# Kernel optimization log

Measured on AMD Instinct MI355X. Metric: run time of the kernel, lower is better.

The kernel has to match this reference:

```python
import jax, jax.numpy as jnp
import numpy as np

B, Hh, Ww, C = 16, 56, 56, 384
HEADS, WS, SHIFT = 12, 7, 3
N = WS * WS            # 49 tokens per window
NW = (Hh // WS) * (Ww // WS)  # 64 windows
HID = int(C * 4.0)
SCALE = (C // HEADS) ** -0.5
EPS = 1e-5


def _relative_position_index():
    coords = np.stack(np.meshgrid(np.arange(WS), np.arange(WS), indexing='ij')).reshape(2, -1)
    rel = (coords[:, :, None] - coords[:, None, :]).transpose(1, 2, 0)  # (N,N,2)
    rel[..., 0] += WS - 1
    rel[..., 1] += WS - 1
    rel[..., 0] *= 2 * WS - 1
    return jnp.asarray(rel.sum(-1))  # (N,N) int

RPI = _relative_position_index()


def _swin_mask():
    img = np.zeros((Hh, Ww), np.float32)
    slices = (slice(0, -WS), slice(-WS, -SHIFT), slice(-SHIFT, None))
    cnt = 0
    for hs in slices:
        for ws in slices:
            img[hs, ws] = cnt
            cnt += 1
    m = img.reshape(Hh // WS, WS, Ww // WS, WS).transpose(0, 2, 1, 3).reshape(-1, N)  # (nW,N)
    am = m[:, None, :] - m[:, :, None]
    return jnp.asarray(np.where(am != 0, -100.0, 0.0).astype(np.float32))  # (nW,N,N)


def setup_inputs() -> dict:
    key = jax.random.key(0)
    ks = jax.random.split(key, 12)
    p = lambda k, shp, s=0.02: (jax.random.normal(k, shp, jnp.float32) * s)
    return {
        'x': jax.random.normal(ks[0], (B, Hh * Ww, C), jnp.float32),
        'mask_matrix': _swin_mask(),
        'norm1_g': jnp.ones((C,), jnp.float32),
        'norm1_b': jnp.zeros((C,), jnp.float32),
        'qkv_w': p(ks[1], (3 * C, C)),
        'qkv_b': jnp.zeros((3 * C,), jnp.float32),
        'rpb_table': p(ks[2], ((2 * WS - 1) * (2 * WS - 1), HEADS)),
        'proj_w': p(ks[3], (C, C)),
        'proj_b': jnp.zeros((C,), jnp.float32),
        'norm2_g': jnp.ones((C,), jnp.float32),
        'norm2_b': jnp.zeros((C,), jnp.float32),
        'fc1_w': p(ks[4], (HID, C)),
        'fc1_b': jnp.zeros((HID,), jnp.float32),
        'fc2_w': p(ks[5], (C, HID)),
        'fc2_b': jnp.zeros((C,), jnp.float32),
    }


def _ln(x, g, b):
    m = jnp.mean(x, -1, keepdims=True)
    v = jnp.mean(jnp.square(x - m), -1, keepdims=True)
    return (x - m) * jax.lax.rsqrt(v + EPS) * g + b


def reference(x, mask_matrix, norm1_g, norm1_b, qkv_w, qkv_b, rpb_table,
              proj_w, proj_b, norm2_g, norm2_b, fc1_w, fc1_b, fc2_w, fc2_b):
    shortcut = x
    h = _ln(x, norm1_g, norm1_b).reshape(B, Hh, Ww, C)
    # cyclic shift (H,W divisible by window -> no pad)
    h = jnp.roll(h, (-SHIFT, -SHIFT), axis=(1, 2))
    # window partition -> (B*nW, N, C)
    win = h.reshape(B, Hh // WS, WS, Ww // WS, WS, C).transpose(0, 1, 3, 2, 4, 5).reshape(-1, N, C)
    B_ = win.shape[0]
    hd = C // HEADS
    qkv = (win @ qkv_w.T + qkv_b).reshape(B_, N, 3, HEADS, hd).transpose(2, 0, 3, 1, 4)
    q, k, v = qkv[0] * SCALE, qkv[1], qkv[2]  # (B_,H,N,hd)
    attn = jnp.einsum('bhnd,bhmd->bhnm', q, k)  # (B_,H,N,N)
    bias = rpb_table[RPI]  # (N,N,heads)
    attn = attn + bias.transpose(2, 0, 1)[None]
    attn = attn.reshape(B, NW, HEADS, N, N) + mask_matrix[None, :, None]
    attn = jax.nn.softmax(attn.reshape(B_, HEADS, N, N), axis=-1)
    out = jnp.einsum('bhnm,bhmd->bhnd', attn, v).transpose(0, 2, 1, 3).reshape(B_, N, C)
    out = out @ proj_w.T + proj_b
    # window reverse + reverse shift
    out = out.reshape(B, Hh // WS, Ww // WS, WS, WS, C).transpose(0, 1, 3, 2, 4, 5).reshape(B, Hh, Ww, C)
    out = jnp.roll(out, (SHIFT, SHIFT), axis=(1, 2)).reshape(B, Hh * Ww, C)
    x = shortcut + out
    h2 = _ln(x, norm2_g, norm2_b)
    h2 = jax.nn.gelu(h2 @ fc1_w.T + fc1_b, approximate=False)  # torch nn.GELU exact
    return x + (h2 @ fc2_w.T + fc2_b)
```

## Files before the change

kernel.cpp:

```cpp
#include <hip/hip_runtime.h>

typedef unsigned short u16;
typedef unsigned int u32;
typedef short s16x8 __attribute__((ext_vector_type(8)));
typedef unsigned short u16x4 __attribute__((ext_vector_type(4)));
typedef float f32x4 __attribute__((ext_vector_type(4)));

#define ATTN_SCALE 0.17677669529663687f

__device__ __forceinline__ u16 f2bf(float f) {
  union { float f; u32 i; } c; c.f = f;
  u32 r = c.i + 0x7fffu + ((c.i >> 16) & 1u);
  return (u16)(r >> 16);
}
__device__ __forceinline__ float bf2f(u16 u) {
  union { u32 i; float f; } c; c.i = ((u32)u) << 16; return c.f;
}
__device__ __forceinline__ f32x4 mfma16(s16x8 a, s16x8 b, f32x4 c) {
  return __builtin_amdgcn_mfma_f32_16x16x32_bf16(a, b, c, 0, 0, 0);
}

typedef __attribute__((address_space(1))) u32 gas_u32;
typedef __attribute__((address_space(3))) u32 las_u32;
#define GLL16(gp, lp) __builtin_amdgcn_global_load_lds((gas_u32*)(gp), (las_u32*)(lp), 16, 0, 0)

__device__ __forceinline__ int win_to_orig(int m) {
  int b = m / 3136, rem = m - b * 3136;
  int w = rem / 49, n = rem - w * 49;
  int wh = w >> 3, ww = w & 7;
  int i = n / 7, j = n - i * 7;
  int r = wh * 7 + i + 3; if (r >= 56) r -= 56;
  int c = ww * 7 + j + 3; if (c >= 56) c -= 56;
  return b * 3136 + r * 56 + c;
}

__global__ __launch_bounds__(256) void cvt_all_kernel(
    const float* __restrict__ qkvw, const float* __restrict__ projw,
    const float* __restrict__ fc1w, const float* __restrict__ fc2w,
    u16* __restrict__ wq, u16* __restrict__ wp,
    u16* __restrict__ w1, u16* __restrict__ w2) {
  int i = blockIdx.x * 256 + threadIdx.x;
  if (i < 442368) wq[i] = f2bf(qkvw[i]);
  else if (i < 589824) wp[i - 442368] = f2bf(projw[i - 442368]);
  else if (i < 1179648) w1[i - 589824] = f2bf(fc1w[i - 589824]);
  else if (i < 1769472) w2[i - 1179648] = f2bf(fc2w[i - 1179648]);
}

__global__ __launch_bounds__(256) void mk_tbl_kernel(
    const float* __restrict__ rpb, const float* __restrict__ maskp,
    u16* __restrict__ tbl) {
  int idx = blockIdx.x * 256 + threadIdx.x;
  int wh = idx >> 12;
  int rem = idx & 4095;
  int irow = rem >> 6;
  int lr = (rem >> 2) & 15, ni = rem & 3;
  int j = ni * 16 + lr;
  int wi = wh / 12, h = wh - wi * 12;
  float val = -1e30f;
  if (irow < 49 && j < 49) {
    int yi = irow / 7, xi = irow - yi * 7;
    int yj = j / 7, xj = j - yj * 7;
    int rpi = (yi - yj + 6) * 13 + (xi - xj + 6);
    val = rpb[rpi * 12 + h] + maskp[((size_t)wi * 49 + irow) * 49 + j];
  }
  tbl[idx] = f2bf(val);
}

template <bool PERM, bool BFIN>
__global__ __launch_bounds__(256) void ln_kernel(
    const void* __restrict__ xin, const float* __restrict__ g,
    const float* __restrict__ bb, u16* __restrict__ xo) {
  int t = blockIdx.x * 4 + (threadIdx.x >> 6);
  int l = threadIdx.x & 63;
  int src = PERM ? win_to_orig(t) : t;
  float v[6];
  if (BFIN) {
    const u16* row = (const u16*)xin + (size_t)src * 384;
#pragma unroll
    for (int k = 0; k < 6; k++) v[k] = bf2f(row[l + 64 * k]);
  } else {
    const float* row = (const float*)xin + (size_t)src * 384;
#pragma unroll
    for (int k = 0; k < 6; k++) v[k] = row[l + 64 * k];
  }
  float s = 0.f;
#pragma unroll
  for (int k = 0; k < 6; k++) s += v[k];
#pragma unroll
  for (int d = 1; d < 64; d <<= 1) s += __shfl_xor(s, d);
  float mean = s * (1.f / 384.f);
  float q = 0.f;
#pragma unroll
  for (int k = 0; k < 6; k++) { float dv = v[k] - mean; q += dv * dv; }
#pragma unroll
  for (int d = 1; d < 64; d <<= 1) q += __shfl_xor(q, d);
  float rstd = rsqrtf(q * (1.f / 384.f) + 1e-5f);
  u16* orow = xo + (size_t)t * 384;
#pragma unroll
  for (int k = 0; k < 6; k++) {
    int c = l + 64 * k;
    orow[c] = f2bf((v[k] - mean) * rstd * g[c] + bb[c]);
  }
}

template <int EPI>
__global__ __launch_bounds__(256) void gemm_kernel(
    const u16* __restrict__ A, const u16* __restrict__ W,
    const float* __restrict__ bias, u16* __restrict__ outb,
    float* __restrict__ outf, const float* __restrict__ auxf,
    const u16* __restrict__ auxb, int K, int N, int NT, int NB) {
  __shared__ __align__(16) short As[8192];
  __shared__ __align__(16) short Bs[8192];
  const int tid = threadIdx.x, wv = tid >> 6, l = tid & 63;
  const int lr = l & 15, lg = l >> 4;
  int bm, bn;
  {
    const int STS = NT << 3;
    const int body = (NB >> 3) * STS;
    int d = blockIdx.x;
    if (d < body) {
      int st = d / STS, rem = d - st * STS;
      bn = rem >> 3;
      bm = st * 8 + (rem & 7);
    } else {
      int t = d - body;
      int tq = t / NT;
      bm = (NB & ~7) + tq;
      bn = t - tq * NT;
    }
  }
  const size_t m0 = (size_t)bm * 128, n0 = (size_t)bn * 128;
  const int prow = wv * 16 + (l >> 2);
  const int ccl = (((l & 3) ^ ((l >> 3) & 3)) << 3);
  const u16* ga0 = A + (m0 + prow) * K + ccl;
  const u16* ga1 = A + (m0 + 64 + prow) * K + ccl;
  const u16* gb0 = W + (n0 + prow) * K + ccl;
  const u16* gb1 = W + (n0 + 64 + prow) * K + ccl;
  const int stoff = wv * 512;
  const int wr = wv >> 1, wc = wv & 1;
  const int sw = (lr >> 1) & 3;
  const int aoff = (wr * 64 + lr) * 32 + ((lg ^ sw) << 3);
  const int boff = (wc * 64 + lr) * 32 + ((lg ^ sw) << 3);

#define STAGE(bufo, koff)                            \
  do {                                               \
    GLL16(ga0 + (koff), As + (bufo) + stoff);        \
    GLL16(ga1 + (koff), As + (bufo) + 2048 + stoff); \
    GLL16(gb0 + (koff), Bs + (bufo) + stoff);        \
    GLL16(gb1 + (koff), Bs + (bufo) + 2048 + stoff); \
  } while (0)
#define FRAG_READS(cur)                                              \
  do {                                                               \
    const short* as = As + (cur);                                    \
    const short* bs = Bs + (cur);                                    \
    _Pragma("unroll") for (int mi = 0; mi < 4; mi++)                 \
        af[mi] = *(const s16x8*)&as[aoff + mi * (16 * 32)];          \
    _Pragma("unroll") for (int ni = 0; ni < 4; ni++)                 \
        bfr[ni] = *(const s16x8*)&bs[boff + ni * (16 * 32)];         \
  } while (0)
#define MFMA_TILE()                                        \
  do {                                                     \
    _Pragma("unroll") for (int mi = 0; mi < 4; mi++)       \
        _Pragma("unroll") for (int ni = 0; ni < 4; ni++)   \
            acc[mi][ni] = mfma16(af[mi], bfr[ni], acc[mi][ni]); \
  } while (0)

  f32x4 acc[4][4] = {};
  s16x8 af[4], bfr[4];
  STAGE(0, 0);
  STAGE(4096, 32);
  int cur = 0;
  int k0 = 0;
  for (; k0 < K - 32; k0 += 32) {
    asm volatile("s_waitcnt vmcnt(4)" ::: "memory");
    __builtin_amdgcn_sched_barrier(0);
    __builtin_amdgcn_s_barrier();
    FRAG_READS(cur);
    asm volatile("s_waitcnt lgkmcnt(0)" ::: "memory");
    __builtin_amdgcn_sched_barrier(0);
    __builtin_amdgcn_s_barrier();
    if (k0 + 64 < K) STAGE(cur, k0 + 64);
    MFMA_TILE();
    cur ^= 4096;
  }
  asm volatile("s_waitcnt vmcnt(0)" ::: "memory");
  __builtin_amdgcn_sched_barrier(0);
  __builtin_amdgcn_s_barrier();
  FRAG_READS(cur);
  asm volatile("s_waitcnt lgkmcnt(0)" ::: "memory");
  __builtin_amdgcn_sched_barrier(0);
  MFMA_TILE();
#undef STAGE
#undef FRAG_READS
#undef MFMA_TILE

  const int colb = (int)n0 + wc * 64;
#pragma unroll
  for (int mi = 0; mi < 4; mi++) {
#pragma unroll
    for (int r = 0; r < 4; r++) {
      const size_t m = m0 + wr * 64 + mi * 16 + lg * 4 + r;
      int dst = 0;
      if (EPI == 1) dst = win_to_orig((int)m);
#pragma unroll
      for (int ni = 0; ni < 4; ni++) {
        const int col = colb + ni * 16 + lr;
        float v = acc[mi][ni][r] + bias[col];
        if (EPI == 0) {
          outb[m * (size_t)N + col] = f2bf(v);
        } else if (EPI == 1) {
          outb[(size_t)dst * 384 + col] = f2bf(v + auxf[(size_t)dst * 384 + col]);
        } else if (EPI == 2) {
          float u = v * (0.7978845608028654f + 0.0356774081f * v * v);
          float gl = v / (1.f + __expf(-2.f * u));
          outb[m * (size_t)N + col] = f2bf(gl);
        } else {
          outf[m * (size_t)N + col] = v + bf2f(auxb[m * (size_t)N + col]);
        }
      }
    }
  }
}

__global__ __launch_bounds__(256) void attn_kernel(
    const u16* __restrict__ qkv, const u16* __restrict__ tbl,
    u16* __restrict__ out) {
  __shared__ __align__(16) short Pl[4][16 * 76];
  const int tid = threadIdx.x, wv = tid >> 6, l = tid & 63;
  const int lr = l & 15, lg = l >> 4;

  const int task = blockIdx.x * 4 + wv;
  const int win = task / 12, h = task - win * 12;
  const int wi = win & 63;
  const short* base = (const short*)qkv + (size_t)win * 49 * 1152 + h * 32;
  const u16* tb = tbl + (size_t)(wi * 12 + h) * 4096 + lr * 4;

  s16x8 qf[4], kf[4];
  const s16x8 zz = {0, 0, 0, 0, 0, 0, 0, 0};
#pragma unroll
  for (int mi = 0; mi < 4; mi++) {
    int n = mi * 16 + lr;
    if (n < 49) {
      qf[mi] = *(const s16x8*)(base + (size_t)n * 1152 + lg * 8);
      kf[mi] = *(const s16x8*)(base + (size_t)n * 1152 + 384 + lg * 8);
    } else { qf[mi] = zz; kf[mi] = zz; }
  }
  s16x8 vb[2][2];
#pragma unroll
  for (int kk = 0; kk < 2; kk++)
#pragma unroll
    for (int nd = 0; nd < 2; nd++)
#pragma unroll
      for (int e = 0; e < 8; e++)
        vb[kk][nd][e] = base[(size_t)(kk * 32 + lg * 8 + e) * 1152 + 768 + nd * 16 + lr];
  u16x4 t4[4][4];
#pragma unroll
  for (int r = 0; r < 4; r++)
    t4[0][r] = *(const u16x4*)&tb[(lg * 4 + r) * 64];

  f32x4 acc[4][4] = {};
  __builtin_amdgcn_s_setprio(1);
#pragma unroll
  for (int mi = 0; mi < 4; mi++)
#pragma unroll
    for (int ni = 0; ni < 4; ni++)
      acc[mi][ni] = mfma16(qf[mi], kf[ni], acc[mi][ni]);
  __builtin_amdgcn_s_setprio(0);

  short* pl = Pl[wv];
#pragma unroll
  for (int mi = 0; mi < 4; mi++) {
    if (mi < 3) {
#pragma unroll
      for (int r = 0; r < 4; r++)
        t4[mi + 1][r] = *(const u16x4*)&tb[((mi + 1) * 16 + lg * 4 + r) * 64];
    }
    float rs[4];
#pragma unroll
    for (int r = 0; r < 4; r++) {
      float sv[4];
#pragma unroll
      for (int ni = 0; ni < 4; ni++)
        sv[ni] = acc[mi][ni][r] * ATTN_SCALE + bf2f(t4[mi][r][ni]);
      float mx = fmaxf(fmaxf(sv[0], sv[1]), fmaxf(sv[2], sv[3]));
#pragma unroll
      for (int d = 1; d < 16; d <<= 1) mx = fmaxf(mx, __shfl_xor(mx, d));
      float sm = 0.f;
#pragma unroll
      for (int ni = 0; ni < 4; ni++) { sv[ni] = __expf(sv[ni] - mx); sm += sv[ni]; }
#pragma unroll
      for (int d = 1; d < 16; d <<= 1) sm += __shfl_xor(sm, d);
      rs[r] = 1.f / sm;
#pragma unroll
      for (int ni = 0; ni < 4; ni++)
        pl[(lg * 4 + r) * 76 + ni * 16 + lr] = (short)f2bf(sv[ni]);
    }
    f32x4 o[2] = {{}, {}};
    __builtin_amdgcn_s_setprio(1);
#pragma unroll
    for (int kk = 0; kk < 2; kk++) {
      s16x8 pa = *(const s16x8*)&pl[lr * 76 + kk * 32 + lg * 8];
#pragma unroll
      for (int nd = 0; nd < 2; nd++)
        o[nd] = mfma16(pa, vb[kk][nd], o[nd]);
    }
    __builtin_amdgcn_s_setprio(0);
#pragma unroll
    for (int r = 0; r < 4; r++) {
      const int irow = mi * 16 + lg * 4 + r;
      if (irow < 49) {
#pragma unroll
        for (int nd = 0; nd < 2; nd++)
          out[((size_t)win * 49 + irow) * 384 + h * 32 + nd * 16 + lr] =
              f2bf(o[nd][r] * rs[r]);
      }
    }
  }
}

extern "C" void kernel_launch(void* const* d_in, const int* in_sizes, int n_in,
                              void* d_out, int out_size, void* d_ws, size_t ws_size,
                              hipStream_t stream) {
  (void)in_sizes; (void)n_in; (void)out_size; (void)ws_size;
  const float* x     = (const float*)d_in[0];
  const float* maskp = (const float*)d_in[1];
  const float* n1g   = (const float*)d_in[2];
  const float* n1b   = (const float*)d_in[3];
  const float* qkvw  = (const float*)d_in[4];
  const float* qkvb  = (const float*)d_in[5];
  const float* rpb   = (const float*)d_in[6];
  const float* projw = (const float*)d_in[7];
  const float* projb = (const float*)d_in[8];
  const float* n2g   = (const float*)d_in[9];
  const float* n2b   = (const float*)d_in[10];
  const float* fc1w  = (const float*)d_in[11];
  const float* fc1b  = (const float*)d_in[12];
  const float* fc2w  = (const float*)d_in[13];
  const float* fc2b  = (const float*)d_in[14];
  float* outp = (float*)d_out;

  char* ws = (char*)d_ws;
  u16*  regA  = (u16*)ws;
  u16*  regB  = (u16*)(ws + 115605504ull);
  u16*  xresb = (u16*)(ws + 154140672ull);
  u16*  wq = (u16*)(ws + 192675840ull);
  u16*  wp = wq + 442368;
  u16*  w1 = wp + 147456;
  u16*  w2 = w1 + 589824;
  u16*  tbl = w2 + 589824;

  cvt_all_kernel<<<6912, 256, 0, stream>>>(qkvw, projw, fc1w, fc2w, wq, wp, w1, w2);
  mk_tbl_kernel<<<12288, 256, 0, stream>>>(rpb, maskp, tbl);
  ln_kernel<true, false><<<12544, 256, 0, stream>>>(x, n1g, n1b, regB);
  gemm_kernel<0><<<392 * 9, 256, 0, stream>>>(regB, wq, qkvb, regA, nullptr,
                                              nullptr, nullptr, 384, 1152, 9, 392);
  attn_kernel<<<3072, 256, 0, stream>>>(regA, tbl, regB);
  gemm_kernel<1><<<392 * 3, 256, 0, stream>>>(regB, wp, projb, xresb, nullptr,
                                              x, nullptr, 384, 384, 3, 392);
  ln_kernel<false, true><<<12544, 256, 0, stream>>>(xresb, n2g, n2b, regB);
  for (int c = 0; c < 2; c++) {
    const u16* aln = regB + (size_t)c * 25088 * 384;
    float* oc = outp + (size_t)c * 25088 * 384;
    const u16* rc = xresb + (size_t)c * 25088 * 384;
    gemm_kernel<2><<<196 * 12, 256, 0, stream>>>(aln, w1, fc1b, regA, nullptr,
                                                 nullptr, nullptr, 384, 1536, 12, 196);
    gemm_kernel<3><<<196 * 3, 256, 0, stream>>>(regA, w2, fc2b, nullptr, oc,
                                                nullptr, rc, 1536, 384, 3, 196);
  }
}
```

Baseline: 409.4 us.

## Add 256x128 GEMM tile variant and run MLP in one pass

Adds a 512-thread GEMM kernel with a 256x128 output tile (8x2 MFMA fragments per wave, setprio around the MFMA block). It is used for the QKV and FC1 GEMMs, while the proj and FC2 GEMMs keep the 128x128 kernel. The workspace is re-laid-out so the FC1 intermediate for all 50176 tokens fits, which removes the two-chunk MLP loop and halves the GEMM launch count there. The bias table and xresb now share a workspace offset, which is safe only because the table is dead after attention. The larger tile raises per-block reuse and register pressure but leaves fewer blocks per GEMM.

```diff
diff --git a/kernel.cpp b/kernel.cpp
--- a/kernel.cpp
+++ b/kernel.cpp
@@ -104,7 +104,25 @@
 }
 
 template <int EPI>
-__global__ __launch_bounds__(256) void gemm_kernel(
+__device__ __forceinline__ void gemm_epi(
+    float v, size_t m, int col, int N, int dst,
+    u16* __restrict__ outb, float* __restrict__ outf,
+    const float* __restrict__ auxf, const u16* __restrict__ auxb) {
+  if (EPI == 0) {
+    outb[m * (size_t)N + col] = f2bf(v);
+  } else if (EPI == 1) {
+    outb[(size_t)dst * 384 + col] = f2bf(v + auxf[(size_t)dst * 384 + col]);
+  } else if (EPI == 2) {
+    float u = v * (0.7978845608028654f + 0.0356774081f * v * v);
+    float gl = v / (1.f + __expf(-2.f * u));
+    outb[m * (size_t)N + col] = f2bf(gl);
+  } else {
+    outf[m * (size_t)N + col] = v + bf2f(auxb[m * (size_t)N + col]);
+  }
+}
+
+template <int EPI>
+__global__ __launch_bounds__(256) void gemm128_kernel(
     const u16* __restrict__ A, const u16* __restrict__ W,
     const float* __restrict__ bias, u16* __restrict__ outb,
     float* __restrict__ outf, const float* __restrict__ auxf,
@@ -154,9 +172,9 @@
     const short* as = As + (cur);                                    \
     const short* bs = Bs + (cur);                                    \
     _Pragma("unroll") for (int mi = 0; mi < 4; mi++)                 \
-        af[mi] = *(const s16x8*)&as[aoff + mi * (16 * 32)];          \
+        af[mi] = *(const s16x8*)&as[aoff + mi * 512];                \
     _Pragma("unroll") for (int ni = 0; ni < 4; ni++)                 \
-        bfr[ni] = *(const s16x8*)&bs[boff + ni * (16 * 32)];         \
+        bfr[ni] = *(const s16x8*)&bs[boff + ni * 512];               \
   } while (0)
 #define MFMA_TILE()                                        \
   do {                                                     \
@@ -205,18 +223,117 @@
 #pragma unroll
       for (int ni = 0; ni < 4; ni++) {
         const int col = colb + ni * 16 + lr;
-        float v = acc[mi][ni][r] + bias[col];
-        if (EPI == 0) {
-          outb[m * (size_t)N + col] = f2bf(v);
-        } else if (EPI == 1) {
-          outb[(size_t)dst * 384 + col] = f2bf(v + auxf[(size_t)dst * 384 + col]);
-        } else if (EPI == 2) {
-          float u = v * (0.7978845608028654f + 0.0356774081f * v * v);
-          float gl = v / (1.f + __expf(-2.f * u));
-          outb[m * (size_t)N + col] = f2bf(gl);
-        } else {
-          outf[m * (size_t)N + col] = v + bf2f(auxb[m * (size_t)N + col]);
-        }
+        gemm_epi<EPI>(acc[mi][ni][r] + bias[col], m, col, N, dst,
+                      outb, outf, auxf, auxb);
+      }
+    }
+  }
+}
+
+template <int EPI>
+__global__ __launch_bounds__(512) void gemm256_kernel(
+    const u16* __restrict__ A, const u16* __restrict__ W,
+    const float* __restrict__ bias, u16* __restrict__ outb,
+    float* __restrict__ outf, const float* __restrict__ auxf,
+    const u16* __restrict__ auxb, int K, int N, int NT, int NB) {
+  __shared__ __align__(16) short As[16384];
+  __shared__ __align__(16) short Bs[8192];
+  const int tid = threadIdx.x, wv = tid >> 6, l = tid & 63;
+  const int lr = l & 15, lg = l >> 4;
+  int bm, bn;
+  {
+    const int STS = NT << 3;
+    const int body = (NB >> 3) * STS;
+    int d = blockIdx.x;
+    if (d < body) {
+      int st = d / STS, rem = d - st * STS;
+      bn = rem >> 3;
+      bm = st * 8 + (rem & 7);
+    } else {
+      int t = d - body;
+      int tq = t / NT;
+      bm = (NB & ~7) + tq;
+      bn = t - tq * NT;
+    }
+  }
+  const size_t m0 = (size_t)bm * 256, n0 = (size_t)bn * 128;
+  const int prow = wv * 16 + (l >> 2);
+  const int ccl = (((l & 3) ^ ((l >> 3) & 3)) << 3);
+  const u16* ga0 = A + (m0 + prow) * K + ccl;
+  const u16* ga1 = A + (m0 + 128 + prow) * K + ccl;
+  const u16* gb0 = W + (n0 + prow) * K + ccl;
+  const int stoff = wv * 512;
+  const int wr = wv >> 2, wc = wv & 3;
+  const int sw = (lr >> 1) & 3;
+  const int aoff = (wr * 128 + lr) * 32 + ((lg ^ sw) << 3);
+  const int boff = (wc * 32 + lr) * 32 + ((lg ^ sw) << 3);
+
+#define STAGE(c, koff)                                     \
+  do {                                                     \
+    GLL16(ga0 + (koff), As + (c) * 8192 + stoff);          \
+    GLL16(ga1 + (koff), As + (c) * 8192 + 4096 + stoff);   \
+    GLL16(gb0 + (koff), Bs + (c) * 4096 + stoff);          \
+  } while (0)
+#define FRAG_READS(c)                                                \
+  do {                                                               \
+    const short* as = As + (c) * 8192;                               \
+    const short* bs = Bs + (c) * 4096;                               \
+    _Pragma("unroll") for (int mi = 0; mi < 8; mi++)                 \
+        af[mi] = *(const s16x8*)&as[aoff + mi * 512];                \
+    _Pragma("unroll") for (int ni = 0; ni < 2; ni++)                 \
+        bfr[ni] = *(const s16x8*)&bs[boff + ni * 512];               \
+  } while (0)
+#define MFMA_TILE()                                        \
+  do {                                                     \
+    __builtin_amdgcn_s_setprio(1);                         \
+    _Pragma("unroll") for (int mi = 0; mi < 8; mi++)       \
+        _Pragma("unroll") for (int ni = 0; ni < 2; ni++)   \
+            acc[mi][ni] = mfma16(af[mi], bfr[ni], acc[mi][ni]); \
+    __builtin_amdgcn_s_setprio(0);                         \
+  } while (0)
+
+  f32x4 acc[8][2] = {};
+  s16x8 af[8], bfr[2];
+  STAGE(0, 0);
+  STAGE(1, 32);
+  int cur = 0;
+  int k0 = 0;
+  for (; k0 < K - 32; k0 += 32) {
+    asm volatile("s_waitcnt vmcnt(3)" ::: "memory");
+    __builtin_amdgcn_sched_barrier(0);
+    __builtin_amdgcn_s_barrier();
+    FRAG_READS(cur);
+    asm volatile("s_waitcnt lgkmcnt(0)" ::: "memory");
+    __builtin_amdgcn_sched_barrier(0);
+    __builtin_amdgcn_s_barrier();
+    if (k0 + 64 < K) STAGE(cur, k0 + 64);
+    MFMA_TILE();
+    cur ^= 1;
+  }
+  asm volatile("s_waitcnt vmcnt(0)" ::: "memory");
+  __builtin_amdgcn_sched_barrier(0);
+  __builtin_amdgcn_s_barrier();
+  FRAG_READS(cur);
+  asm volatile("s_waitcnt lgkmcnt(0)" ::: "memory");
+  __builtin_amdgcn_sched_barrier(0);
+  MFMA_TILE();
+#undef STAGE
+#undef FRAG_READS
+#undef MFMA_TILE
+
+  const int colb = (int)n0 + wc * 32;
+#pragma unroll
+  for (int mi = 0; mi < 8; mi++) {
+#pragma unroll
+    for (int r = 0; r < 4; r++) {
+      const size_t m = m0 + wr * 128 + mi * 16 + lg * 4 + r;
+      int dst = 0;
+      if (EPI == 1) dst = win_to_orig((int)m);
+#pragma unroll
+      for (int ni = 0; ni < 2; ni++) {
+        const int col = colb + ni * 16 + lr;
+        gemm_epi<EPI>(acc[mi][ni][r] + bias[col], m, col, N, dst,
+                      outb, outf, auxf, auxb);
       }
     }
   }
@@ -341,30 +458,25 @@
 
   char* ws = (char*)d_ws;
   u16*  regA  = (u16*)ws;
-  u16*  regB  = (u16*)(ws + 115605504ull);
-  u16*  xresb = (u16*)(ws + 154140672ull);
-  u16*  wq = (u16*)(ws + 192675840ull);
+  u16*  regB  = (u16*)(ws + 154140672ull);
+  u16*  tbl   = (u16*)(ws + 192675840ull);
+  u16*  xresb = (u16*)(ws + 192675840ull);
+  u16*  wq = (u16*)(ws + 231211008ull);
   u16*  wp = wq + 442368;
   u16*  w1 = wp + 147456;
   u16*  w2 = w1 + 589824;
-  u16*  tbl = w2 + 589824;
 
   cvt_all_kernel<<<6912, 256, 0, stream>>>(qkvw, projw, fc1w, fc2w, wq, wp, w1, w2);
   mk_tbl_kernel<<<12288, 256, 0, stream>>>(rpb, maskp, tbl);
   ln_kernel<true, false><<<12544, 256, 0, stream>>>(x, n1g, n1b, regB);
-  gemm_kernel<0><<<392 * 9, 256, 0, stream>>>(regB, wq, qkvb, regA, nullptr,
-                                              nullptr, nullptr, 384, 1152, 9, 392);
+  gemm256_kernel<0><<<196 * 9, 512, 0, stream>>>(regB, wq, qkvb, regA, nullptr,
+                                                 nullptr, nullptr, 384, 1152, 9, 196);
   attn_kernel<<<3072, 256, 0, stream>>>(regA, tbl, regB);
-  gemm_kernel<1><<<392 * 3, 256, 0, stream>>>(regB, wp, projb, xresb, nullptr,
-                                              x, nullptr, 384, 384, 3, 392);
+  gemm128_kernel<1><<<392 * 3, 256, 0, stream>>>(regB, wp, projb, xresb, nullptr,
+                                                 x, nullptr, 384, 384, 3, 392);
   ln_kernel<false, true><<<12544, 256, 0, stream>>>(xresb, n2g, n2b, regB);
-  for (int c = 0; c < 2; c++) {
-    const u16* aln = regB + (size_t)c * 25088 * 384;
-    float* oc = outp + (size_t)c * 25088 * 384;
-    const u16* rc = xresb + (size_t)c * 25088 * 384;
-    gemm_kernel<2><<<196 * 12, 256, 0, stream>>>(aln, w1, fc1b, regA, nullptr,
-                                                 nullptr, nullptr, 384, 1536, 12, 196);
-    gemm_kernel<3><<<196 * 3, 256, 0, stream>>>(regA, w2, fc2b, nullptr, oc,
-                                                nullptr, rc, 1536, 384, 3, 196);
-  }
-}
+  gemm256_kernel<2><<<196 * 12, 512, 0, stream>>>(regB, w1, fc1b, regA, nullptr,
+                                                  nullptr, nullptr, 384, 1536, 12, 196);
+  gemm128_kernel<3><<<392 * 3, 256, 0, stream>>>(regA, w2, fc2b, nullptr, outp,
+                                                 nullptr, xresb, 1536, 384, 3, 392);
+}
```

New measurement: 406.6 us, median of 2. Within noise of the previous version (-0.7%).
